# Optimization experiments

Measured on AMD Instinct MI355X. Metric: run time of the kernel, lower is better.

Reference implementation:

```python
import jax, jax.numpy as jnp
import numpy as np
import math

N_HEADS, INPUT_DIM, EMBED_DIM = 8, 512, 512
KEY_DIM = EMBED_DIM // N_HEADS  # val_dim == key_dim == 64
B, NQ, G = 4, 2048, 2048


def setup_inputs() -> dict:
    key = jax.random.key(0)
    ks = jax.random.split(key, 7)
    stdv_k = 1.0 / math.sqrt(KEY_DIM)
    stdv_e = 1.0 / math.sqrt(EMBED_DIM)
    return {
        "q": jax.random.normal(ks[0], (B, NQ, INPUT_DIM), jnp.float32),
        "h": jax.random.normal(ks[1], (B, G, INPUT_DIM), jnp.float32),
        "mask": jax.random.randint(ks[2], (B, NQ, G), 0, 2) == 1,  # True = attention not possible
        "W_query": jax.random.uniform(ks[3], (N_HEADS, INPUT_DIM, KEY_DIM), jnp.float32, -stdv_k, stdv_k),
        "W_key": jax.random.uniform(ks[4], (N_HEADS, INPUT_DIM, KEY_DIM), jnp.float32, -stdv_k, stdv_k),
        "W_val": jax.random.uniform(ks[5], (N_HEADS, INPUT_DIM, KEY_DIM), jnp.float32, -stdv_k, stdv_k),
        "W_out": jax.random.uniform(ks[6], (N_HEADS, KEY_DIM, EMBED_DIM), jnp.float32, -stdv_e, stdv_e),
    }


def reference(q, h, mask, W_query, W_key, W_val, W_out):
    norm = 1.0 / math.sqrt(KEY_DIM)
    # Per-head projections: (H, B, S, kd)
    Q = jnp.einsum("bqd,hdk->hbqk", q, W_query)
    K = jnp.einsum("bgd,hdk->hbgk", h, W_key)
    V = jnp.einsum("bgd,hdv->hbgv", h, W_val)
    # Full attention scores: (H, B, NQ, G)
    comp = norm * jnp.einsum("hbqk,hbgk->hbqg", Q, K)
    m = mask[None]  # (1, B, NQ, G) broadcasts over heads
    comp = jnp.where(m, -jnp.inf, comp)
    attn = jax.nn.softmax(comp, axis=-1)
    attn = jnp.where(m, 0.0, attn)  # mirrors the clone + zero step (also fixes all-masked rows)
    heads = jnp.einsum("hbqg,hbgv->hbqv", attn, V)
    # Output projection: flatten heads and apply W_out (H, vd, E)
    out = jnp.einsum("hbqv,hve->bqe", heads, W_out)
    return out
```

## Files before the change

### kernel.cpp

```cpp
#include <hip/hip_runtime.h>
#include <hip/hip_bf16.h>
#include <stdint.h>

#define NHEADS 8
#define INDIM 512
#define EMB 512
#define BSZ 4
#define NQS 2048
#define GS 2048

#define ALPHA_F 0.18033688011112042f

#if __has_builtin(__builtin_amdgcn_exp2f)
#define EXP2(x) __builtin_amdgcn_exp2f(x)
#else
#define EXP2(x) __expf((x)*0.69314718056f)
#endif

typedef short bf16x8 __attribute__((ext_vector_type(8)));
typedef float f32x4 __attribute__((ext_vector_type(4)));
typedef float f32x16 __attribute__((ext_vector_type(16)));
typedef unsigned int u32x4 __attribute__((ext_vector_type(4)));

static __device__ __forceinline__ unsigned short f2bf(float f) {
  unsigned int u = __builtin_bit_cast(unsigned int, f);
  unsigned int rounding = 0x7FFFu + ((u >> 16) & 1u);
  u += rounding;
  return (unsigned short)(u >> 16);
}

typedef __attribute__((address_space(3))) void lds_void;
typedef __attribute__((address_space(1))) const void gm_void;
static __device__ __forceinline__ void gll16(const void* g, void* s) {
  __builtin_amdgcn_global_load_lds((gm_void*)g, (lds_void*)s, 16, 0, 0);
}

__global__ void k_prep(const float4* __restrict__ q, const float4* __restrict__ h,
                       const void* __restrict__ mask,
                       const float* __restrict__ wq, const float* __restrict__ wk,
                       const float* __restrict__ wv, const float* __restrict__ wo,
                       ushort4* __restrict__ qb, ushort4* __restrict__ hb,
                       unsigned short* __restrict__ wqt, unsigned short* __restrict__ wkvt,
                       unsigned short* __restrict__ wot, unsigned short* __restrict__ maskB16) {
  int blk = blockIdx.x, t = threadIdx.x;
  if (blk < 2048) {
    const float4* src = blk < 1024 ? q : h;
    ushort4* dst = blk < 1024 ? qb : hb;
    int base = (blk & 1023) * 256 + t;
#pragma unroll
    for (int i = 0; i < 4; i++) {
      int idx = base + i * 262144;
      float4 v = src[idx];
      ushort4 o;
      o.x = f2bf(v.x); o.y = f2bf(v.y); o.z = f2bf(v.z); o.w = f2bf(v.w);
      dst[idx] = o;
    }
  } else if (blk < 3072) {
    const unsigned int* m32h = (const unsigned int*)mask;
    bool bytes = __ballot(m32h[t & 63] > 1u) != 0ull;
    int base = (blk - 2048) * 256 + t;
#pragma unroll
    for (int i = 0; i < 4; i++) {
      int widx = base + i * 262144;
      unsigned int bits = 0;
      if (bytes) {
        const uchar4* p = (const uchar4*)((const unsigned char*)mask + (size_t)widx * 16);
#pragma unroll
        for (int j = 0; j < 4; j++) {
          uchar4 v = p[j];
          bits |= ((v.x ? 1u : 0u) << (4 * j)) | ((v.y ? 1u : 0u) << (4 * j + 1)) |
                  ((v.z ? 1u : 0u) << (4 * j + 2)) | ((v.w ? 1u : 0u) << (4 * j + 3));
        }
      } else {
        const int4* p = (const int4*)((const int*)mask + (size_t)widx * 16);
#pragma unroll
        for (int j = 0; j < 4; j++) {
          int4 v = p[j];
          bits |= ((v.x ? 1u : 0u) << (4 * j)) | ((v.y ? 1u : 0u) << (4 * j + 1)) |
                  ((v.z ? 1u : 0u) << (4 * j + 2)) | ((v.w ? 1u : 0u) << (4 * j + 3));
        }
      }
      maskB16[widx] = (unsigned short)bits;
    }
  } else {
    int id = (blk - 3072) * 256 + t;
#pragma unroll
    for (int i = 0; i < 8; i++) {
      int e = id * 8 + i;
      int which = e >> 18, r = e & 262143;
      int k = r & 511, n = r >> 9;
      int hh = n >> 6, j = n & 63;
      if (which == 0) wqt[r] = f2bf(wq[hh * 32768 + k * 64 + j] * ALPHA_F);
      else if (which == 1) wkvt[r] = f2bf(wk[hh * 32768 + k * 64 + j]);
      else if (which == 2) wkvt[262144 + r] = f2bf(wv[hh * 32768 + k * 64 + j]);
      else wot[r] = f2bf(wo[k * 512 + n]);
    }
  }
}


__global__ __launch_bounds__(256) void k_gemmQKV2(const unsigned short* __restrict__ qb_,
                                                  const unsigned short* __restrict__ hb_,
                                                  const unsigned short* __restrict__ wqt,
                                                  const unsigned short* __restrict__ wkvt,
                                                  unsigned short* __restrict__ Qp,
                                                  unsigned short* __restrict__ Kp,
                                                  unsigned short* __restrict__ Vt) {
  __shared__ unsigned short As[2][4096];
  __shared__ unsigned short Bs[2][4096];
  int ny = blockIdx.y;
  const unsigned short* A = (ny < 4) ? qb_ : hb_;
  const unsigned short* Bt = (ny < 4) ? wqt : wkvt;
  int n0 = (ny < 4) ? ny * 128 : (ny - 4) * 128;
  int m0 = blockIdx.x * 128;
  int t = threadIdx.x;
  int w = t >> 6, l = t & 63, c = l & 15, lg = l >> 4;
  int wr = w >> 1, wc = w & 1;

  int sRow = (t >> 6) * 16 + (t & 15);
  int sK = ((t >> 4) & 3) * 8;
  const unsigned short* aG = A + (size_t)(m0 + sRow) * 512 + sK;
  const unsigned short* bG = Bt + (size_t)(n0 + sRow) * 512 + sK;
  int ldsOff = t * 16;

  f32x4 acc[4][4];
#pragma unroll
  for (int mi = 0; mi < 4; mi++)
#pragma unroll
    for (int ni = 0; ni < 4; ni++) acc[mi][ni] = {0.f, 0.f, 0.f, 0.f};

  gll16(aG, (char*)As[0] + ldsOff);
  gll16(aG + 64 * 512, (char*)As[0] + ldsOff + 4096);
  gll16(bG, (char*)Bs[0] + ldsOff);
  gll16(bG + 64 * 512, (char*)Bs[0] + ldsOff + 4096);

  for (int kk = 0; kk < 16; kk++) {
    int cur = kk & 1;
    asm volatile("s_waitcnt vmcnt(0)" ::: "memory");
    __builtin_amdgcn_s_barrier();
    if (kk < 15) {
      int ko = (kk + 1) * 32;
      gll16(aG + ko, (char*)As[cur ^ 1] + ldsOff);
      gll16(aG + ko + 64 * 512, (char*)As[cur ^ 1] + ldsOff + 4096);
      gll16(bG + ko, (char*)Bs[cur ^ 1] + ldsOff);
      gll16(bG + ko + 64 * 512, (char*)Bs[cur ^ 1] + ldsOff + 4096);
    }
    bf16x8 af[4], bfr[4];
#pragma unroll
    for (int mi = 0; mi < 4; mi++)
      af[mi] = *(const bf16x8*)((const char*)As[cur] + (((wr * 4 + mi) * 64 + l) * 16));
#pragma unroll
    for (int ni = 0; ni < 4; ni++)
      bfr[ni] = *(const bf16x8*)((const char*)Bs[cur] + (((wc * 4 + ni) * 64 + l) * 16));
#pragma unroll
    for (int mi = 0; mi < 4; mi++)
#pragma unroll
      for (int ni = 0; ni < 4; ni++)
        acc[mi][ni] = __builtin_amdgcn_mfma_f32_16x16x32_bf16(af[mi], bfr[ni], acc[mi][ni], 0, 0, 0);
  }

#pragma unroll
  for (int mi = 0; mi < 4; mi++)
#pragma unroll
    for (int ni = 0; ni < 4; ni++) {
      int row = m0 + wr * 64 + mi * 16 + 4 * lg;
      int col = n0 + wc * 64 + ni * 16 + c;
      if (ny < 4) {
#pragma unroll
        for (int r = 0; r < 4; r++)
          Qp[(size_t)(row + r) * 512 + col] = f2bf(acc[mi][ni][r]);
      } else if (col < 512) {
#pragma unroll
        for (int r = 0; r < 4; r++)
          Kp[(size_t)(row + r) * 512 + col] = f2bf(acc[mi][ni][r]);
      } else {
        int col5 = col - 512, hd2 = col5 >> 6, vv = col5 & 63;
        int bb = row >> 11, g = row & 2047;
        ushort4 u;
        u.x = f2bf(acc[mi][ni][0]);
        u.y = f2bf(acc[mi][ni][1]);
        u.z = f2bf(acc[mi][ni][2]);
        u.w = f2bf(acc[mi][ni][3]);
        *(ushort4*)(Vt + (size_t)((bb * 8 + hd2) * 64 + vv) * GS + g) = u;
      }
    }
}

__global__ __launch_bounds__(256) void k_gemmO(const unsigned short* __restrict__ A,
                                               const unsigned short* __restrict__ Bt,
                                               float* __restrict__ C) {
  __shared__ unsigned short As[2][4096];
  __shared__ unsigned short Bs[2][4096];
  int m0 = blockIdx.x * 128, n0 = blockIdx.y * 128;
  int t = threadIdx.x;
  int w = t >> 6, l = t & 63, c = l & 15, lg = l >> 4;
  int wr = w >> 1, wc = w & 1;

  int sRow = (t >> 6) * 16 + (t & 15);
  int sK = ((t >> 4) & 3) * 8;
  const unsigned short* aG = A + (size_t)(m0 + sRow) * 512 + sK;
  const unsigned short* bG = Bt + (size_t)(n0 + sRow) * 512 + sK;
  int ldsOff = t * 16;

  f32x4 acc[4][4];
#pragma unroll
  for (int mi = 0; mi < 4; mi++)
#pragma unroll
    for (int ni = 0; ni < 4; ni++) acc[mi][ni] = {0.f, 0.f, 0.f, 0.f};

  gll16(aG, (char*)As[0] + ldsOff);
  gll16(aG + 64 * 512, (char*)As[0] + ldsOff + 4096);
  gll16(bG, (char*)Bs[0] + ldsOff);
  gll16(bG + 64 * 512, (char*)Bs[0] + ldsOff + 4096);

  for (int kk = 0; kk < 16; kk++) {
    int cur = kk & 1;
    asm volatile("s_waitcnt vmcnt(0)" ::: "memory");
    __builtin_amdgcn_s_barrier();
    if (kk < 15) {
      int ko = (kk + 1) * 32;
      gll16(aG + ko, (char*)As[cur ^ 1] + ldsOff);
      gll16(aG + ko + 64 * 512, (char*)As[cur ^ 1] + ldsOff + 4096);
      gll16(bG + ko, (char*)Bs[cur ^ 1] + ldsOff);
      gll16(bG + ko + 64 * 512, (char*)Bs[cur ^ 1] + ldsOff + 4096);
    }
    bf16x8 af[4], bfr[4];
#pragma unroll
    for (int mi = 0; mi < 4; mi++)
      af[mi] = *(const bf16x8*)((const char*)As[cur] + (((wr * 4 + mi) * 64 + l) * 16));
#pragma unroll
    for (int ni = 0; ni < 4; ni++)
      bfr[ni] = *(const bf16x8*)((const char*)Bs[cur] + (((wc * 4 + ni) * 64 + l) * 16));
#pragma unroll
    for (int mi = 0; mi < 4; mi++)
#pragma unroll
      for (int ni = 0; ni < 4; ni++)
        acc[mi][ni] = __builtin_amdgcn_mfma_f32_16x16x32_bf16(af[mi], bfr[ni], acc[mi][ni], 0, 0, 0);
  }

#pragma unroll
  for (int mi = 0; mi < 4; mi++)
#pragma unroll
    for (int ni = 0; ni < 4; ni++) {
      int row = m0 + wr * 64 + mi * 16 + 4 * lg;
      int col = n0 + wc * 64 + ni * 16 + c;
#pragma unroll
      for (int r = 0; r < 4; r++)
        C[(size_t)(row + r) * 512 + col] = acc[mi][ni][r];
    }
}

__global__ __launch_bounds__(256, 2) void k_attn10(const unsigned short* __restrict__ Qp,
                                                   const unsigned short* __restrict__ Kp,
                                                   const unsigned short* __restrict__ Vt,
                                                   const unsigned short* __restrict__ maskB16,
                                                   unsigned short* __restrict__ Hd) {
  __shared__ unsigned short Ksh[2][4096];
  __shared__ unsigned short Vsh[2][4096];

  int bid = blockIdx.x;
  int fid = (bid & 7) * 64 + (bid >> 3);
  int qtile = fid & 15;
  int bh = fid >> 4;
  int b = bh >> 3, hd = bh & 7;

  int t = threadIdx.x;
  int w = t >> 6, l = t & 63;
  int lo = l & 31, hi = l >> 5, hi4 = hi * 4;
  int q = qtile * 128 + w * 32 + lo;

  const unsigned short* qrow = Qp + (size_t)(b * NQS + q) * 512 + hd * 64 + hi * 8;
  bf16x8 qf[4];
#pragma unroll
  for (int s = 0; s < 4; s++) qf[s] = *(const bf16x8*)(qrow + s * 16);

  const unsigned short* kg0 = Kp + (size_t)(b * GS + lo) * 512 + hd * 64 + w * 16 + hi * 8;
  int vbS = (t >> 7) & 1, s2S = (t >> 6) & 1;
  const unsigned short* vg0 = Vt + (size_t)(bh * 64 + vbS * 32 + lo) * GS + s2S * 16 + hi * 8;
  char* kd[2] = {(char*)Ksh[0] + w * 1024, (char*)Ksh[1] + w * 1024};
  char* vd[2] = {(char*)Vsh[0] + w * 1024, (char*)Vsh[1] + w * 1024};

  f32x16 o0, o1;
#pragma unroll
  for (int i = 0; i < 16; i++) { o0[i] = 0.f; o1[i] = 0.f; }
  float ls[4] = {0.f, 0.f, 0.f, 0.f};

  const unsigned long long* mrow = (const unsigned long long*)maskB16 + (size_t)(b * NQS + q) * 32;

  gll16(kg0, kd[0]);
  gll16(kg0 + 32 * 512, kd[0] + 4096);
  gll16(vg0, vd[0]);
  gll16(vg0 + 32, vd[0] + 4096);
  unsigned long long wm = mrow[0], wmn = 0;

  for (int kt = 0; kt < 32; kt++) {
    int cur = kt & 1;
    asm volatile("s_waitcnt vmcnt(0)" ::: "memory");
    __builtin_amdgcn_s_barrier();
    if (kt < 31) {
      const unsigned short* kg = kg0 + (size_t)(kt + 1) * 64 * 512;
      const unsigned short* vg = vg0 + (size_t)(kt + 1) * 64;
      gll16(kg, kd[cur ^ 1]);
      gll16(kg + 32 * 512, kd[cur ^ 1] + 4096);
      gll16(vg, vd[cur ^ 1]);
      gll16(vg + 32, vd[cur ^ 1] + 4096);
      wmn = mrow[kt + 1];
    }

    const unsigned short* Kc = (const unsigned short*)Ksh[cur];
    const unsigned short* Vc = (const unsigned short*)Vsh[cur];

    f32x16 s0, s1;
#pragma unroll
    for (int i = 0; i < 16; i++) { s0[i] = 0.f; s1[i] = 0.f; }
    __builtin_amdgcn_s_setprio(1);
#pragma unroll
    for (int s = 0; s < 4; s++) {
      bf16x8 ka0 = *(const bf16x8*)(Kc + (s * 64 + l) * 8);
      s0 = __builtin_amdgcn_mfma_f32_32x32x16_bf16(ka0, qf[s], s0, 0, 0, 0);
    }
#pragma unroll
    for (int s = 0; s < 4; s++) {
      bf16x8 ka1 = *(const bf16x8*)(Kc + 2048 + (s * 64 + l) * 8);
      s1 = __builtin_amdgcn_mfma_f32_32x32x16_bf16(ka1, qf[s], s1, 0, 0, 0);
    }
    __builtin_amdgcn_s_setprio(0);

    unsigned int mb0 = (unsigned int)wm;
    float p0[16];
#pragma unroll
    for (int r = 0; r < 16; r++) {
      float e = EXP2(s0[r]);
      unsigned bit = (mb0 >> ((r & 3) + 8 * (r >> 2) + hi4)) & 1u;
      p0[r] = bit ? 0.f : e;
      ls[r & 3] += p0[r];
    }
    unsigned int a0, a1, a2, a3, a4, a5, a6, a7;
    asm("v_cvt_pk_bf16_f32 %0, %1, %2" : "=v"(a0) : "v"(p0[0]), "v"(p0[1]));
    asm("v_cvt_pk_bf16_f32 %0, %1, %2" : "=v"(a1) : "v"(p0[2]), "v"(p0[3]));
    asm("v_cvt_pk_bf16_f32 %0, %1, %2" : "=v"(a2) : "v"(p0[4]), "v"(p0[5]));
    asm("v_cvt_pk_bf16_f32 %0, %1, %2" : "=v"(a3) : "v"(p0[6]), "v"(p0[7]));
    asm("v_cvt_pk_bf16_f32 %0, %1, %2" : "=v"(a4) : "v"(p0[8]), "v"(p0[9]));
    asm("v_cvt_pk_bf16_f32 %0, %1, %2" : "=v"(a5) : "v"(p0[10]), "v"(p0[11]));
    asm("v_cvt_pk_bf16_f32 %0, %1, %2" : "=v"(a6) : "v"(p0[12]), "v"(p0[13]));
    asm("v_cvt_pk_bf16_f32 %0, %1, %2" : "=v"(a7) : "v"(p0[14]), "v"(p0[15]));
    asm("v_permlane32_swap_b32 %0, %1" : "+v"(a0), "+v"(a2));
    asm("v_permlane32_swap_b32 %0, %1" : "+v"(a1), "+v"(a3));
    asm("v_permlane32_swap_b32 %0, %1" : "+v"(a4), "+v"(a6));
    asm("v_permlane32_swap_b32 %0, %1" : "+v"(a5), "+v"(a7));
    u32x4 pw00 = {a0, a1, a2, a3};
    u32x4 pw01 = {a4, a5, a6, a7};
    bf16x8 pb00 = __builtin_bit_cast(bf16x8, pw00);
    bf16x8 pb01 = __builtin_bit_cast(bf16x8, pw01);
    {
      bf16x8 va00 = *(const bf16x8*)(Vc + (0 * 64 + l) * 8);
      bf16x8 va01 = *(const bf16x8*)(Vc + (1 * 64 + l) * 8);
      bf16x8 va10 = *(const bf16x8*)(Vc + (2 * 64 + l) * 8);
      bf16x8 va11 = *(const bf16x8*)(Vc + (3 * 64 + l) * 8);
      __builtin_amdgcn_s_setprio(1);
      o0 = __builtin_amdgcn_mfma_f32_32x32x16_bf16(va00, pb00, o0, 0, 0, 0);
      o1 = __builtin_amdgcn_mfma_f32_32x32x16_bf16(va10, pb00, o1, 0, 0, 0);
      o0 = __builtin_amdgcn_mfma_f32_32x32x16_bf16(va01, pb01, o0, 0, 0, 0);
      o1 = __builtin_amdgcn_mfma_f32_32x32x16_bf16(va11, pb01, o1, 0, 0, 0);
      __builtin_amdgcn_s_setprio(0);
    }

    unsigned int mb1 = (unsigned int)(wm >> 32);
    float p1[16];
#pragma unroll
    for (int r = 0; r < 16; r++) {
      float e = EXP2(s1[r]);
      unsigned bit = (mb1 >> ((r & 3) + 8 * (r >> 2) + hi4)) & 1u;
      p1[r] = bit ? 0.f : e;
      ls[r & 3] += p1[r];
    }
    unsigned int b0, b1, b2, b3, b4, b5, b6, b7;
    asm("v_cvt_pk_bf16_f32 %0, %1, %2" : "=v"(b0) : "v"(p1[0]), "v"(p1[1]));
    asm("v_cvt_pk_bf16_f32 %0, %1, %2" : "=v"(b1) : "v"(p1[2]), "v"(p1[3]));
    asm("v_cvt_pk_bf16_f32 %0, %1, %2" : "=v"(b2) : "v"(p1[4]), "v"(p1[5]));
    asm("v_cvt_pk_bf16_f32 %0, %1, %2" : "=v"(b3) : "v"(p1[6]), "v"(p1[7]));
    asm("v_cvt_pk_bf16_f32 %0, %1, %2" : "=v"(b4) : "v"(p1[8]), "v"(p1[9]));
    asm("v_cvt_pk_bf16_f32 %0, %1, %2" : "=v"(b5) : "v"(p1[10]), "v"(p1[11]));
    asm("v_cvt_pk_bf16_f32 %0, %1, %2" : "=v"(b6) : "v"(p1[12]), "v"(p1[13]));
    asm("v_cvt_pk_bf16_f32 %0, %1, %2" : "=v"(b7) : "v"(p1[14]), "v"(p1[15]));
    asm("v_permlane32_swap_b32 %0, %1" : "+v"(b0), "+v"(b2));
    asm("v_permlane32_swap_b32 %0, %1" : "+v"(b1), "+v"(b3));
    asm("v_permlane32_swap_b32 %0, %1" : "+v"(b4), "+v"(b6));
    asm("v_permlane32_swap_b32 %0, %1" : "+v"(b5), "+v"(b7));
    u32x4 pw10 = {b0, b1, b2, b3};
    u32x4 pw11 = {b4, b5, b6, b7};
    bf16x8 pb10 = __builtin_bit_cast(bf16x8, pw10);
    bf16x8 pb11 = __builtin_bit_cast(bf16x8, pw11);
    {
      bf16x8 vb00 = *(const bf16x8*)(Vc + 2048 + (0 * 64 + l) * 8);
      bf16x8 vb01 = *(const bf16x8*)(Vc + 2048 + (1 * 64 + l) * 8);
      bf16x8 vb10 = *(const bf16x8*)(Vc + 2048 + (2 * 64 + l) * 8);
      bf16x8 vb11 = *(const bf16x8*)(Vc + 2048 + (3 * 64 + l) * 8);
      __builtin_amdgcn_s_setprio(1);
      o0 = __builtin_amdgcn_mfma_f32_32x32x16_bf16(vb00, pb10, o0, 0, 0, 0);
      o1 = __builtin_amdgcn_mfma_f32_32x32x16_bf16(vb10, pb10, o1, 0, 0, 0);
      o0 = __builtin_amdgcn_mfma_f32_32x32x16_bf16(vb01, pb11, o0, 0, 0, 0);
      o1 = __builtin_amdgcn_mfma_f32_32x32x16_bf16(vb11, pb11, o1, 0, 0, 0);
      __builtin_amdgcn_s_setprio(0);
    }
    wm = wmn;
  }

  float lsum = (ls[0] + ls[1]) + (ls[2] + ls[3]);
  lsum += __shfl_xor(lsum, 32);
  float inv = lsum > 0.f ? 1.0f / lsum : 0.f;
  unsigned short* hrow = Hd + (size_t)(b * NQS + q) * 512 + hd * 64;
#pragma unroll
  for (int vt = 0; vt < 2; vt++) {
#pragma unroll
    for (int gr = 0; gr < 4; gr++) {
      ushort4 u;
      float v0 = (vt ? o1[gr * 4 + 0] : o0[gr * 4 + 0]) * inv;
      float v1 = (vt ? o1[gr * 4 + 1] : o0[gr * 4 + 1]) * inv;
      float v2 = (vt ? o1[gr * 4 + 2] : o0[gr * 4 + 2]) * inv;
      float v3 = (vt ? o1[gr * 4 + 3] : o0[gr * 4 + 3]) * inv;
      u.x = f2bf(v0); u.y = f2bf(v1); u.z = f2bf(v2); u.w = f2bf(v3);
      int vv = vt * 32 + 8 * gr + hi4;
      *(ushort4*)(hrow + vv) = u;
    }
  }
}


extern "C" void kernel_launch(void* const* d_in, const int* in_sizes, int n_in,
                              void* d_out, int out_size, void* d_ws, size_t ws_size,
                              hipStream_t stream) {
  const float* q = (const float*)d_in[0];
  const float* h = (const float*)d_in[1];
  const void* mask = d_in[2];
  const float* wq = (const float*)d_in[3];
  const float* wk = (const float*)d_in[4];
  const float* wv = (const float*)d_in[5];
  const float* wo = (const float*)d_in[6];
  float* out = (float*)d_out;

  unsigned short* qb_ = (unsigned short*)d_ws;
  unsigned short* hb_ = qb_ + 8192 * 512;
  unsigned short* Qp = hb_ + 8192 * 512;
  unsigned short* Kp = Qp + 8192 * 512;
  unsigned short* Vtp = Kp + 8192 * 512;
  unsigned short* Hd = Vtp + 8192 * 512;
  unsigned short* wqt = Hd + 8192 * 512;
  unsigned short* wkvt = wqt + 512 * 512;
  unsigned short* wot = wkvt + 1024 * 512;
  unsigned short* maskB16 = wot + 512 * 512;

  k_prep<<<3584, 256, 0, stream>>>((const float4*)q, (const float4*)h, mask, wq, wk, wv, wo,
                                   (ushort4*)qb_, (ushort4*)hb_, wqt, wkvt, wot, maskB16);
  dim3 gqkv(64, 12);
  k_gemmQKV2<<<gqkv, 256, 0, stream>>>(qb_, hb_, wqt, wkvt, Qp, Kp, Vtp);
  k_attn10<<<512, 256, 0, stream>>>(Qp, Kp, Vtp, maskB16, Hd);
  dim3 go(64, 4);
  k_gemmO<<<go, 256, 0, stream>>>(Hd, wot, out);
}
```

Before: 132.7 us.

## Overlap mask packing with QKV GEMM and retile output projection GEMM

Mask bit-packing moves out of the prep kernel and into extra blocks of the QKV projection GEMM grid, so the memory-bound mask conversion runs alongside the MFMA work instead of before it. The output projection GEMM is retiled to 64x128 blocks with K-steps of 64, doubling the grid to 512 blocks for better CU occupancy and halving the barrier count. The trade-offs are that the mask blocks now compete with GEMM blocks for bandwidth and CU slots, and the new LDS layout may cause bank conflicts.

```diff
diff --git a/kernel.cpp b/kernel.cpp
--- a/kernel.cpp
+++ b/kernel.cpp
@@ -36,12 +36,11 @@
 }
 
 __global__ void k_prep(const float4* __restrict__ q, const float4* __restrict__ h,
-                       const void* __restrict__ mask,
                        const float* __restrict__ wq, const float* __restrict__ wk,
                        const float* __restrict__ wv, const float* __restrict__ wo,
                        ushort4* __restrict__ qb, ushort4* __restrict__ hb,
                        unsigned short* __restrict__ wqt, unsigned short* __restrict__ wkvt,
-                       unsigned short* __restrict__ wot, unsigned short* __restrict__ maskB16) {
+                       unsigned short* __restrict__ wot) {
   int blk = blockIdx.x, t = threadIdx.x;
   if (blk < 2048) {
     const float4* src = blk < 1024 ? q : h;
@@ -55,35 +54,8 @@
       o.x = f2bf(v.x); o.y = f2bf(v.y); o.z = f2bf(v.z); o.w = f2bf(v.w);
       dst[idx] = o;
     }
-  } else if (blk < 3072) {
-    const unsigned int* m32h = (const unsigned int*)mask;
-    bool bytes = __ballot(m32h[t & 63] > 1u) != 0ull;
-    int base = (blk - 2048) * 256 + t;
-#pragma unroll
-    for (int i = 0; i < 4; i++) {
-      int widx = base + i * 262144;
-      unsigned int bits = 0;
-      if (bytes) {
-        const uchar4* p = (const uchar4*)((const unsigned char*)mask + (size_t)widx * 16);
-#pragma unroll
-        for (int j = 0; j < 4; j++) {
-          uchar4 v = p[j];
-          bits |= ((v.x ? 1u : 0u) << (4 * j)) | ((v.y ? 1u : 0u) << (4 * j + 1)) |
-                  ((v.z ? 1u : 0u) << (4 * j + 2)) | ((v.w ? 1u : 0u) << (4 * j + 3));
-        }
-      } else {
-        const int4* p = (const int4*)((const int*)mask + (size_t)widx * 16);
-#pragma unroll
-        for (int j = 0; j < 4; j++) {
-          int4 v = p[j];
-          bits |= ((v.x ? 1u : 0u) << (4 * j)) | ((v.y ? 1u : 0u) << (4 * j + 1)) |
-                  ((v.z ? 1u : 0u) << (4 * j + 2)) | ((v.w ? 1u : 0u) << (4 * j + 3));
-        }
-      }
-      maskB16[widx] = (unsigned short)bits;
-    }
   } else {
-    int id = (blk - 3072) * 256 + t;
+    int id = (blk - 2048) * 256 + t;
 #pragma unroll
     for (int i = 0; i < 8; i++) {
       int e = id * 8 + i;
@@ -98,22 +70,54 @@
   }
 }
 
-
 __global__ __launch_bounds__(256) void k_gemmQKV2(const unsigned short* __restrict__ qb_,
                                                   const unsigned short* __restrict__ hb_,
                                                   const unsigned short* __restrict__ wqt,
                                                   const unsigned short* __restrict__ wkvt,
+                                                  const void* __restrict__ mask,
+                                                  unsigned short* __restrict__ maskB16,
                                                   unsigned short* __restrict__ Qp,
                                                   unsigned short* __restrict__ Kp,
                                                   unsigned short* __restrict__ Vt) {
   __shared__ unsigned short As[2][4096];
   __shared__ unsigned short Bs[2][4096];
   int ny = blockIdx.y;
+  int t = threadIdx.x;
+
+  if (ny >= 12) {
+    const unsigned int* m32h = (const unsigned int*)mask;
+    bool bytes = __ballot(m32h[t & 63] > 1u) != 0ull;
+    int id = ((ny - 12) * 64 + blockIdx.x) * 256 + t;
+#pragma unroll
+    for (int i = 0; i < 16; i++) {
+      int widx = id + i * 65536;
+      unsigned int bits = 0;
+      if (bytes) {
+        const uchar4* p = (const uchar4*)((const unsigned char*)mask + (size_t)widx * 16);
+#pragma unroll
+        for (int j = 0; j < 4; j++) {
+          uchar4 v = p[j];
+          bits |= ((v.x ? 1u : 0u) << (4 * j)) | ((v.y ? 1u : 0u) << (4 * j + 1)) |
+                  ((v.z ? 1u : 0u) << (4 * j + 2)) | ((v.w ? 1u : 0u) << (4 * j + 3));
+        }
+      } else {
+        const int4* p = (const int4*)((const int*)mask + (size_t)widx * 16);
+#pragma unroll
+        for (int j = 0; j < 4; j++) {
+          int4 v = p[j];
+          bits |= ((v.x ? 1u : 0u) << (4 * j)) | ((v.y ? 1u : 0u) << (4 * j + 1)) |
+                  ((v.z ? 1u : 0u) << (4 * j + 2)) | ((v.w ? 1u : 0u) << (4 * j + 3));
+        }
+      }
+      maskB16[widx] = (unsigned short)bits;
+    }
+    return;
+  }
+
   const unsigned short* A = (ny < 4) ? qb_ : hb_;
   const unsigned short* Bt = (ny < 4) ? wqt : wkvt;
   int n0 = (ny < 4) ? ny * 128 : (ny - 4) * 128;
   int m0 = blockIdx.x * 128;
-  int t = threadIdx.x;
   int w = t >> 6, l = t & 63, c = l & 15, lg = l >> 4;
   int wr = w >> 1, wc = w & 1;
 
@@ -186,63 +190,71 @@
     }
 }
 
-__global__ __launch_bounds__(256) void k_gemmO(const unsigned short* __restrict__ A,
+__global__ __launch_bounds__(256) void k_gemm3(const unsigned short* __restrict__ A,
                                                const unsigned short* __restrict__ Bt,
                                                float* __restrict__ C) {
   __shared__ unsigned short As[2][4096];
-  __shared__ unsigned short Bs[2][4096];
-  int m0 = blockIdx.x * 128, n0 = blockIdx.y * 128;
+  __shared__ unsigned short Bs[2][8192];
+  int m0 = blockIdx.x * 64, n0 = blockIdx.y * 128;
   int t = threadIdx.x;
   int w = t >> 6, l = t & 63, c = l & 15, lg = l >> 4;
   int wr = w >> 1, wc = w & 1;
 
-  int sRow = (t >> 6) * 16 + (t & 15);
-  int sK = ((t >> 4) & 3) * 8;
-  const unsigned short* aG = A + (size_t)(m0 + sRow) * 512 + sK;
-  const unsigned short* bG = Bt + (size_t)(n0 + sRow) * 512 + sK;
-  int ldsOff = t * 16;
-
-  f32x4 acc[4][4];
-#pragma unroll
-  for (int mi = 0; mi < 4; mi++)
+  int rbA = t >> 7, kcc = (t >> 4) & 7, cc = t & 15;
+  const unsigned short* aG = A + (size_t)(m0 + rbA * 16 + cc) * 512 + kcc * 8;
+  const unsigned short* bG = Bt + (size_t)(n0 + rbA * 16 + cc) * 512 + kcc * 8;
+  int ldsOff = w * 1024 + (t & 63) * 16;
+
+  f32x4 acc[2][4];
+#pragma unroll
+  for (int mi = 0; mi < 2; mi++)
 #pragma unroll
     for (int ni = 0; ni < 4; ni++) acc[mi][ni] = {0.f, 0.f, 0.f, 0.f};
 
   gll16(aG, (char*)As[0] + ldsOff);
-  gll16(aG + 64 * 512, (char*)As[0] + ldsOff + 4096);
+  gll16(aG + 32 * 512, (char*)As[0] + ldsOff + 4096);
   gll16(bG, (char*)Bs[0] + ldsOff);
-  gll16(bG + 64 * 512, (char*)Bs[0] + ldsOff + 4096);
-
-  for (int kk = 0; kk < 16; kk++) {
+  gll16(bG + 32 * 512, (char*)Bs[0] + ldsOff + 4096);
+  gll16(bG + 64 * 512, (char*)Bs[0] + ldsOff + 8192);
+  gll16(bG + 96 * 512, (char*)Bs[0] + ldsOff + 12288);
+
+  for (int kk = 0; kk < 8; kk++) {
     int cur = kk & 1;
     asm volatile("s_waitcnt vmcnt(0)" ::: "memory");
     __builtin_amdgcn_s_barrier();
-    if (kk < 15) {
-      int ko = (kk + 1) * 32;
+    if (kk < 7) {
+      int ko = (kk + 1) * 64;
       gll16(aG + ko, (char*)As[cur ^ 1] + ldsOff);
-      gll16(aG + ko + 64 * 512, (char*)As[cur ^ 1] + ldsOff + 4096);
+      gll16(aG + ko + 32 * 512, (char*)As[cur ^ 1] + ldsOff + 4096);
       gll16(bG + ko, (char*)Bs[cur ^ 1] + ldsOff);
-      gll16(bG + ko + 64 * 512, (char*)Bs[cur ^ 1] + ldsOff + 4096);
-    }
-    bf16x8 af[4], bfr[4];
-#pragma unroll
-    for (int mi = 0; mi < 4; mi++)
-      af[mi] = *(const bf16x8*)((const char*)As[cur] + (((wr * 4 + mi) * 64 + l) * 16));
-#pragma unroll
-    for (int ni = 0; ni < 4; ni++)
-      bfr[ni] = *(const bf16x8*)((const char*)Bs[cur] + (((wc * 4 + ni) * 64 + l) * 16));
-#pragma unroll
-    for (int mi = 0; mi < 4; mi++)
+      gll16(bG + ko + 32 * 512, (char*)Bs[cur ^ 1] + ldsOff + 4096);
+      gll16(bG + ko + 64 * 512, (char*)Bs[cur ^ 1] + ldsOff + 8192);
+      gll16(bG + ko + 96 * 512, (char*)Bs[cur ^ 1] + ldsOff + 12288);
+    }
+    bf16x8 af[2][2], bfr[4][2];
+#pragma unroll
+    for (int kc = 0; kc < 2; kc++) {
+#pragma unroll
+      for (int mi = 0; mi < 2; mi++)
+        af[mi][kc] = *(const bf16x8*)((const char*)As[cur] + ((wr * 2 + mi) * 128 + (kc * 4 + lg) * 16 + c) * 16);
 #pragma unroll
       for (int ni = 0; ni < 4; ni++)
-        acc[mi][ni] = __builtin_amdgcn_mfma_f32_16x16x32_bf16(af[mi], bfr[ni], acc[mi][ni], 0, 0, 0);
-  }
-
-#pragma unroll
-  for (int mi = 0; mi < 4; mi++)
+        bfr[ni][kc] = *(const bf16x8*)((const char*)Bs[cur] + ((wc * 4 + ni) * 128 + (kc * 4 + lg) * 16 + c) * 16);
+    }
+#pragma unroll
+    for (int kc = 0; kc < 2; kc++)
+#pragma unroll
+      for (int mi = 0; mi < 2; mi++)
+#pragma unroll
+        for (int ni = 0; ni < 4; ni++)
+          acc[mi][ni] = __builtin_amdgcn_mfma_f32_16x16x32_bf16(af[mi][kc], bfr[ni][kc], acc[mi][ni], 0, 0, 0);
+  }
+
+#pragma unroll
+  for (int mi = 0; mi < 2; mi++)
 #pragma unroll
     for (int ni = 0; ni < 4; ni++) {
-      int row = m0 + wr * 64 + mi * 16 + 4 * lg;
+      int row = m0 + wr * 32 + mi * 16 + 4 * lg;
       int col = n0 + wc * 64 + ni * 16 + c;
 #pragma unroll
       for (int r = 0; r < 4; r++)
@@ -450,11 +462,11 @@
   unsigned short* wot = wkvt + 1024 * 512;
   unsigned short* maskB16 = wot + 512 * 512;
 
-  k_prep<<<3584, 256, 0, stream>>>((const float4*)q, (const float4*)h, mask, wq, wk, wv, wo,
-                                   (ushort4*)qb_, (ushort4*)hb_, wqt, wkvt, wot, maskB16);
-  dim3 gqkv(64, 12);
-  k_gemmQKV2<<<gqkv, 256, 0, stream>>>(qb_, hb_, wqt, wkvt, Qp, Kp, Vtp);
+  k_prep<<<2560, 256, 0, stream>>>((const float4*)q, (const float4*)h, wq, wk, wv, wo,
+                                   (ushort4*)qb_, (ushort4*)hb_, wqt, wkvt, wot);
+  dim3 gqkv(64, 16);
+  k_gemmQKV2<<<gqkv, 256, 0, stream>>>(qb_, hb_, wqt, wkvt, mask, maskB16, Qp, Kp, Vtp);
   k_attn10<<<512, 256, 0, stream>>>(Qp, Kp, Vtp, maskB16, Hd);
-  dim3 go(64, 4);
-  k_gemmO<<<go, 256, 0, stream>>>(Hd, wot, out);
-}
+  dim3 go(128, 4);
+  k_gemm3<<<go, 256, 0, stream>>>(Hd, wot, out);
+}
```

New measurement: 133.5 us. About the same (+0.6%).
